# Performance work log

Hardware: AMD Instinct MI355X
Metric: run time of the kernel (lower is better)

## Reference

```python
import jax, jax.numpy as jnp
import numpy as np

N_NODES = 100000
N_EDGES = 1000000
D = 172          # n_node_features == memory_dimension (added together)
B = 4096         # batch after src/dst concat
K = 20           # n_neighbors


def setup_inputs() -> dict:
    key = jax.random.key(0)
    ks = jax.random.split(key, 12)
    return {
        "node_feats": jax.random.normal(ks[0], (N_NODES, D), dtype=jnp.float32),
        "edge_feats": jax.random.normal(ks[1], (N_EDGES, D), dtype=jnp.float32),
        "memory": jax.random.normal(ks[2], (N_NODES, D), dtype=jnp.float32),
        "timestamps": jax.random.uniform(ks[3], (B,), dtype=jnp.float32),
        "edge_times1": jax.random.uniform(ks[4], (B, K), dtype=jnp.float32),
        "edge_times2": jax.random.uniform(ks[5], (B * K, K), dtype=jnp.float32),
        "source_nodes": jax.random.randint(ks[6], (B,), 0, N_NODES),
        "neighbors1": jax.random.randint(ks[7], (B, K), 0, N_NODES),
        "edge_idxs1": jax.random.randint(ks[8], (B, K), 0, N_EDGES),
        "neighbors2": jax.random.randint(ks[9], (B * K, K), 0, N_NODES),
        "edge_idxs2": jax.random.randint(ks[10], (B * K, K), 0, N_EDGES),
    }


def reference(node_feats, edge_feats, memory, timestamps, edge_times1,
              edge_times2, source_nodes, neighbors1, edge_idxs1,
              neighbors2, edge_idxs2):
    # node_features[idx] + memory[idx] == (node_features + memory)[idx]
    node_mem = node_feats + memory  # [N, D]

    # ---- layer 0 data_collect ----
    src_feats1 = node_mem[source_nodes]        # [B, D]
    neigh_feats1 = node_mem[neighbors1]        # [B, K, D]
    edge_f1 = edge_feats[edge_idxs1]           # [B, K, D]
    deltas1 = timestamps[:, None] - edge_times1  # [B, K]
    mask1 = neighbors1 == 0                    # [B, K]

    # ---- layer 1 data_collect: nodes = neighbors.flatten(), ts repeated ----
    nodes2 = neighbors1.reshape(-1)            # [B*K]
    ts2 = jnp.repeat(timestamps, K)            # [B*K]
    src_feats2 = node_mem[nodes2]              # [B*K, D]
    neigh_feats2 = node_mem[neighbors2]        # [B*K, K, D]
    edge_f2 = edge_feats[edge_idxs2]           # [B*K, K, D]
    deltas2 = ts2[:, None] - edge_times2       # [B*K, K]
    mask2 = neighbors2 == 0                    # [B*K, K]

    return (src_feats1, neigh_feats1, edge_f1, deltas1, mask1,
            src_feats2, neigh_feats2, edge_f2, deltas2, mask2)
```

## Files before the change

### kernel.cpp

```cpp
#include <hip/hip_runtime.h>

typedef float f32x4 __attribute__((ext_vector_type(4)));

static constexpr unsigned D4 = 43;

__device__ __forceinline__ void nt_store4(f32x4* p, f32x4 v) {
    __builtin_nontemporal_store(v, p);
}

__global__ void addtab_k(f32x4* __restrict__ dst,
                         const f32x4* __restrict__ a,
                         const f32x4* __restrict__ b,
                         unsigned n4) {
    unsigned i = blockIdx.x * blockDim.x + threadIdx.x;
    unsigned stride = gridDim.x * blockDim.x;
    for (; i < n4; i += stride) {
        dst[i] = a[i] + b[i];
    }
}

__global__ void gather4_k(f32x4* __restrict__ dst,
                          const f32x4* __restrict__ a,
                          const int* __restrict__ idx,
                          unsigned n4) {
    unsigned i = blockIdx.x * blockDim.x + threadIdx.x;
    unsigned stride = gridDim.x * blockDim.x;
    for (; i < n4; i += stride) {
        unsigned row = i / D4;
        unsigned col = i - row * D4;
        unsigned s   = (unsigned)idx[row] * D4 + col;
        nt_store4(dst + i, a[s]);
    }
}

__global__ void gather4_dual_k(f32x4* __restrict__ dst1,
                               f32x4* __restrict__ dst2,
                               const f32x4* __restrict__ a,
                               const int* __restrict__ idx,
                               unsigned n4) {
    unsigned i = blockIdx.x * blockDim.x + threadIdx.x;
    unsigned stride = gridDim.x * blockDim.x;
    for (; i < n4; i += stride) {
        unsigned row = i / D4;
        unsigned col = i - row * D4;
        unsigned s   = (unsigned)idx[row] * D4 + col;
        f32x4 v = a[s];
        nt_store4(dst1 + i, v);
        nt_store4(dst2 + i, v);
    }
}

__global__ void gather_add4_k(f32x4* __restrict__ dst,
                              const f32x4* __restrict__ a,
                              const f32x4* __restrict__ b,
                              const int* __restrict__ idx,
                              unsigned n4) {
    unsigned i = blockIdx.x * blockDim.x + threadIdx.x;
    unsigned stride = gridDim.x * blockDim.x;
    for (; i < n4; i += stride) {
        unsigned row = i / D4;
        unsigned col = i - row * D4;
        unsigned s   = (unsigned)idx[row] * D4 + col;
        nt_store4(dst + i, a[s] + b[s]);
    }
}

__global__ void gather_add4_dual_k(f32x4* __restrict__ dst1,
                                   f32x4* __restrict__ dst2,
                                   const f32x4* __restrict__ a,
                                   const f32x4* __restrict__ b,
                                   const int* __restrict__ idx,
                                   unsigned n4) {
    unsigned i = blockIdx.x * blockDim.x + threadIdx.x;
    unsigned stride = gridDim.x * blockDim.x;
    for (; i < n4; i += stride) {
        unsigned row = i / D4;
        unsigned col = i - row * D4;
        unsigned s   = (unsigned)idx[row] * D4 + col;
        f32x4 v = a[s] + b[s];
        nt_store4(dst1 + i, v);
        nt_store4(dst2 + i, v);
    }
}

template <unsigned TSD>
__global__ void dm_k(float* __restrict__ deltas,
                     float* __restrict__ mask,
                     const float* __restrict__ ts,
                     const float* __restrict__ et,
                     const int* __restrict__ neigh,
                     unsigned n) {
    unsigned i = blockIdx.x * blockDim.x + threadIdx.x;
    unsigned stride = gridDim.x * blockDim.x;
    for (; i < n; i += stride) {
        __builtin_nontemporal_store(ts[i / TSD] - et[i], deltas + i);
        __builtin_nontemporal_store((neigh[i] == 0) ? 1.0f : 0.0f, mask + i);
    }
}

static inline unsigned grid_for(unsigned n, unsigned block, unsigned cap) {
    unsigned g = (n + block - 1) / block;
    return g < cap ? (g ? g : 1) : cap;
}

extern "C" void kernel_launch(void* const* d_in, const int* in_sizes, int n_in,
                              void* d_out, int out_size, void* d_ws, size_t ws_size,
                              hipStream_t stream) {
    const float* nf  = (const float*)d_in[0];
    const float* ef  = (const float*)d_in[1];
    const float* mem = (const float*)d_in[2];
    const float* ts  = (const float*)d_in[3];
    const float* et1 = (const float*)d_in[4];
    const float* et2 = (const float*)d_in[5];
    const int* srcn  = (const int*)d_in[6];
    const int* nb1   = (const int*)d_in[7];
    const int* ei1   = (const int*)d_in[8];
    const int* nb2   = (const int*)d_in[9];
    const int* ei2   = (const int*)d_in[10];

    constexpr unsigned B = 4096, K = 20, Dd = 172;
    constexpr unsigned BK = B * K;
    constexpr unsigned NN = 100000;

    float* out = (float*)d_out;
    size_t o = 0;
    float* src1 = out + o;  o += (size_t)B * Dd;
    float* nf1  = out + o;  o += (size_t)BK * Dd;
    float* ef1  = out + o;  o += (size_t)BK * Dd;
    float* dl1  = out + o;  o += (size_t)BK;
    float* mk1  = out + o;  o += (size_t)BK;
    float* sf2  = out + o;  o += (size_t)BK * Dd;
    float* nf2  = out + o;  o += (size_t)BK * K * Dd;
    float* ef2  = out + o;  o += (size_t)BK * K * Dd;
    float* dl2  = out + o;  o += (size_t)BK * K;
    float* mk2  = out + o;  o += (size_t)BK * K;

    const f32x4* nf4  = (const f32x4*)nf;
    const f32x4* mem4 = (const f32x4*)mem;
    const f32x4* ef4  = (const f32x4*)ef;

    const unsigned BLK = 256;
    const unsigned CAP = 2048;

    const size_t NM_BYTES = (size_t)NN * Dd * sizeof(float);

    if (ws_size >= NM_BYTES) {
        f32x4* nm4 = (f32x4*)d_ws;
        {
            unsigned n4 = NN * D4;
            addtab_k<<<grid_for(n4, BLK, CAP), BLK, 0, stream>>>(nm4, nf4, mem4, n4);
        }
        {
            unsigned n4 = B * D4;
            gather4_k<<<grid_for(n4, BLK, CAP), BLK, 0, stream>>>(
                (f32x4*)src1, nm4, srcn, n4);
        }
        {
            unsigned n4 = BK * D4;
            gather4_dual_k<<<grid_for(n4, BLK, CAP), BLK, 0, stream>>>(
                (f32x4*)nf1, (f32x4*)sf2, nm4, nb1, n4);
        }
        {
            unsigned n4 = BK * K * D4;
            gather4_k<<<grid_for(n4, BLK, CAP), BLK, 0, stream>>>(
                (f32x4*)nf2, nm4, nb2, n4);
        }
        dm_k<K><<<grid_for(BK, BLK, CAP), BLK, 0, stream>>>(dl1, mk1, ts, et1, nb1, BK);
        dm_k<K * K><<<grid_for(BK * K, BLK, CAP), BLK, 0, stream>>>(
            dl2, mk2, ts, et2, nb2, BK * K);
        {
            unsigned n4 = BK * D4;
            gather4_k<<<grid_for(n4, BLK, CAP), BLK, 0, stream>>>(
                (f32x4*)ef1, ef4, ei1, n4);
        }
        {
            unsigned n4 = BK * K * D4;
            gather4_k<<<grid_for(n4, BLK, CAP), BLK, 0, stream>>>(
                (f32x4*)ef2, ef4, ei2, n4);
        }
    } else {
        {
            unsigned n4 = B * D4;
            gather_add4_k<<<grid_for(n4, BLK, CAP), BLK, 0, stream>>>(
                (f32x4*)src1, nf4, mem4, srcn, n4);
        }
        {
            unsigned n4 = BK * D4;
            gather_add4_dual_k<<<grid_for(n4, BLK, CAP), BLK, 0, stream>>>(
                (f32x4*)nf1, (f32x4*)sf2, nf4, mem4, nb1, n4);
        }
        {
            unsigned n4 = BK * K * D4;
            gather_add4_k<<<grid_for(n4, BLK, CAP), BLK, 0, stream>>>(
                (f32x4*)nf2, nf4, mem4, nb2, n4);
        }
        dm_k<K><<<grid_for(BK, BLK, CAP), BLK, 0, stream>>>(dl1, mk1, ts, et1, nb1, BK);
        dm_k<K * K><<<grid_for(BK * K, BLK, CAP), BLK, 0, stream>>>(
            dl2, mk2, ts, et2, nb2, BK * K);
        {
            unsigned n4 = BK * D4;
            gather4_k<<<grid_for(n4, BLK, CAP), BLK, 0, stream>>>(
                (f32x4*)ef1, ef4, ei1, n4);
        }
        {
            unsigned n4 = BK * K * D4;
            gather4_k<<<grid_for(n4, BLK, CAP), BLK, 0, stream>>>(
                (f32x4*)ef2, ef4, ei2, n4);
        }
    }
}
```

Measured before the change: 804.8 us.

## Fuse independent stages into three block-partitioned kernels with exact grids

Replaces eight launches with three. The first kernel partitions its blocks across the node+memory table add, both delta/mask computations and the layer-1 edge gather. The second does all node-table gathers and the third does the large edge gather. Each uses one element per thread with exact grid sizes instead of capped grid-stride loops. This removes launch gaps and tail idle time and lets independent work overlap, but it relies on hardcoded problem sizes dividing evenly by 256 and removes the bounds checks.

```diff
diff --git a/kernel.cpp b/kernel.cpp
--- a/kernel.cpp
+++ b/kernel.cpp
@@ -4,20 +4,81 @@
 
 static constexpr unsigned D4 = 43;
 
-__device__ __forceinline__ void nt_store4(f32x4* p, f32x4 v) {
-    __builtin_nontemporal_store(v, p);
-}
-
-__global__ void addtab_k(f32x4* __restrict__ dst,
-                         const f32x4* __restrict__ a,
-                         const f32x4* __restrict__ b,
-                         unsigned n4) {
-    unsigned i = blockIdx.x * blockDim.x + threadIdx.x;
-    unsigned stride = gridDim.x * blockDim.x;
-    for (; i < n4; i += stride) {
-        dst[i] = a[i] + b[i];
-    }
-}
+
+__global__ __launch_bounds__(256) void k1_fused(
+    f32x4* __restrict__ nm, const f32x4* __restrict__ nf, const f32x4* __restrict__ mem,
+    float* __restrict__ dl1, float* __restrict__ mk1, const float* __restrict__ ts,
+    const float* __restrict__ et1, const int* __restrict__ nb1,
+    float* __restrict__ dl2, float* __restrict__ mk2,
+    const float* __restrict__ et2, const int* __restrict__ nb2,
+    f32x4* __restrict__ ef1o, const f32x4* __restrict__ ef, const int* __restrict__ ei1)
+{
+    constexpr unsigned ADD_N = 100000u * D4;
+    constexpr unsigned ADD_B = (ADD_N + 255u) / 256u;
+    constexpr unsigned DM1_B = 81920u / 256u;
+    constexpr unsigned DM2_B = 1638400u / 256u;
+    unsigned b = blockIdx.x, t = threadIdx.x;
+
+    if (b < ADD_B) {
+        unsigned i = b * 256u + t;
+        if (i < ADD_N) nm[i] = nf[i] + mem[i];
+    } else if (b < ADD_B + DM1_B) {
+        unsigned i = (b - ADD_B) * 256u + t;
+        __builtin_nontemporal_store(ts[i / 20u] - et1[i], dl1 + i);
+        __builtin_nontemporal_store((nb1[i] == 0) ? 1.0f : 0.0f, mk1 + i);
+    } else if (b < ADD_B + DM1_B + DM2_B) {
+        unsigned i = (b - ADD_B - DM1_B) * 256u + t;
+        __builtin_nontemporal_store(ts[i / 400u] - et2[i], dl2 + i);
+        __builtin_nontemporal_store((nb2[i] == 0) ? 1.0f : 0.0f, mk2 + i);
+    } else {
+        unsigned i = (b - ADD_B - DM1_B - DM2_B) * 256u + t;
+        unsigned row = i / D4, col = i - row * D4;
+        unsigned s = (unsigned)ei1[row] * D4 + col;
+        __builtin_nontemporal_store(ef[s], ef1o + i);
+    }
+}
+static constexpr unsigned K1_BLOCKS =
+    ((100000u * 43u + 255u) / 256u) + (81920u / 256u) + (1638400u / 256u)
+    + ((81920u * 43u) / 256u);
+
+__global__ __launch_bounds__(256) void k2_nodes(
+    const f32x4* __restrict__ nm,
+    f32x4* __restrict__ src1, const int* __restrict__ srcn,
+    f32x4* __restrict__ nf1o, f32x4* __restrict__ sf2, const int* __restrict__ nb1,
+    f32x4* __restrict__ nf2o, const int* __restrict__ nb2)
+{
+    constexpr unsigned S1_B = (4096u * D4) / 256u;
+    constexpr unsigned N1_B = (81920u * D4) / 256u;
+    unsigned b = blockIdx.x, t = threadIdx.x;
+
+    if (b < S1_B) {
+        unsigned i = b * 256u + t;
+        unsigned row = i / D4, col = i - row * D4;
+        __builtin_nontemporal_store(nm[(unsigned)srcn[row] * D4 + col], src1 + i);
+    } else if (b < S1_B + N1_B) {
+        unsigned i = (b - S1_B) * 256u + t;
+        unsigned row = i / D4, col = i - row * D4;
+        f32x4 v = nm[(unsigned)nb1[row] * D4 + col];
+        __builtin_nontemporal_store(v, nf1o + i);
+        __builtin_nontemporal_store(v, sf2 + i);
+    } else {
+        unsigned i = (b - S1_B - N1_B) * 256u + t;
+        unsigned row = i / D4, col = i - row * D4;
+        __builtin_nontemporal_store(nm[(unsigned)nb2[row] * D4 + col], nf2o + i);
+    }
+}
+static constexpr unsigned K2_BLOCKS =
+    ((4096u * 43u) / 256u) + ((81920u * 43u) / 256u) + ((1638400u * 43u) / 256u);
+
+__global__ __launch_bounds__(256) void k3_ef2(
+    f32x4* __restrict__ dst, const f32x4* __restrict__ ef, const int* __restrict__ ei2)
+{
+    unsigned i = blockIdx.x * 256u + threadIdx.x;
+    unsigned row = i / D4, col = i - row * D4;
+    __builtin_nontemporal_store(ef[(unsigned)ei2[row] * D4 + col], dst + i);
+}
+static constexpr unsigned K3_BLOCKS = (1638400u * 43u) / 256u;
+
 
 __global__ void gather4_k(f32x4* __restrict__ dst,
                           const f32x4* __restrict__ a,
@@ -26,27 +87,8 @@
     unsigned i = blockIdx.x * blockDim.x + threadIdx.x;
     unsigned stride = gridDim.x * blockDim.x;
     for (; i < n4; i += stride) {
-        unsigned row = i / D4;
-        unsigned col = i - row * D4;
-        unsigned s   = (unsigned)idx[row] * D4 + col;
-        nt_store4(dst + i, a[s]);
-    }
-}
-
-__global__ void gather4_dual_k(f32x4* __restrict__ dst1,
-                               f32x4* __restrict__ dst2,
-                               const f32x4* __restrict__ a,
-                               const int* __restrict__ idx,
-                               unsigned n4) {
-    unsigned i = blockIdx.x * blockDim.x + threadIdx.x;
-    unsigned stride = gridDim.x * blockDim.x;
-    for (; i < n4; i += stride) {
-        unsigned row = i / D4;
-        unsigned col = i - row * D4;
-        unsigned s   = (unsigned)idx[row] * D4 + col;
-        f32x4 v = a[s];
-        nt_store4(dst1 + i, v);
-        nt_store4(dst2 + i, v);
+        unsigned row = i / D4, col = i - row * D4;
+        __builtin_nontemporal_store(a[(unsigned)idx[row] * D4 + col], dst + i);
     }
 }
 
@@ -58,10 +100,9 @@
     unsigned i = blockIdx.x * blockDim.x + threadIdx.x;
     unsigned stride = gridDim.x * blockDim.x;
     for (; i < n4; i += stride) {
-        unsigned row = i / D4;
-        unsigned col = i - row * D4;
-        unsigned s   = (unsigned)idx[row] * D4 + col;
-        nt_store4(dst + i, a[s] + b[s]);
+        unsigned row = i / D4, col = i - row * D4;
+        unsigned s = (unsigned)idx[row] * D4 + col;
+        __builtin_nontemporal_store(a[s] + b[s], dst + i);
     }
 }
 
@@ -74,12 +115,11 @@
     unsigned i = blockIdx.x * blockDim.x + threadIdx.x;
     unsigned stride = gridDim.x * blockDim.x;
     for (; i < n4; i += stride) {
-        unsigned row = i / D4;
-        unsigned col = i - row * D4;
-        unsigned s   = (unsigned)idx[row] * D4 + col;
+        unsigned row = i / D4, col = i - row * D4;
+        unsigned s = (unsigned)idx[row] * D4 + col;
         f32x4 v = a[s] + b[s];
-        nt_store4(dst1 + i, v);
-        nt_store4(dst2 + i, v);
+        __builtin_nontemporal_store(v, dst1 + i);
+        __builtin_nontemporal_store(v, dst2 + i);
     }
 }
 
@@ -139,31 +179,37 @@
     const f32x4* mem4 = (const f32x4*)mem;
     const f32x4* ef4  = (const f32x4*)ef;
 
-    const unsigned BLK = 256;
-    const unsigned CAP = 2048;
-
     const size_t NM_BYTES = (size_t)NN * Dd * sizeof(float);
 
     if (ws_size >= NM_BYTES) {
         f32x4* nm4 = (f32x4*)d_ws;
-        {
-            unsigned n4 = NN * D4;
-            addtab_k<<<grid_for(n4, BLK, CAP), BLK, 0, stream>>>(nm4, nf4, mem4, n4);
-        }
+        k1_fused<<<K1_BLOCKS, 256, 0, stream>>>(
+            nm4, nf4, mem4,
+            dl1, mk1, ts, et1, nb1,
+            dl2, mk2, et2, nb2,
+            (f32x4*)ef1, ef4, ei1);
+        k2_nodes<<<K2_BLOCKS, 256, 0, stream>>>(
+            nm4,
+            (f32x4*)src1, srcn,
+            (f32x4*)nf1, (f32x4*)sf2, nb1,
+            (f32x4*)nf2, nb2);
+        k3_ef2<<<K3_BLOCKS, 256, 0, stream>>>((f32x4*)ef2, ef4, ei2);
+    } else {
+        const unsigned BLK = 256, CAP = 2048;
         {
             unsigned n4 = B * D4;
-            gather4_k<<<grid_for(n4, BLK, CAP), BLK, 0, stream>>>(
-                (f32x4*)src1, nm4, srcn, n4);
+            gather_add4_k<<<grid_for(n4, BLK, CAP), BLK, 0, stream>>>(
+                (f32x4*)src1, nf4, mem4, srcn, n4);
         }
         {
             unsigned n4 = BK * D4;
-            gather4_dual_k<<<grid_for(n4, BLK, CAP), BLK, 0, stream>>>(
-                (f32x4*)nf1, (f32x4*)sf2, nm4, nb1, n4);
+            gather_add4_dual_k<<<grid_for(n4, BLK, CAP), BLK, 0, stream>>>(
+                (f32x4*)nf1, (f32x4*)sf2, nf4, mem4, nb1, n4);
         }
         {
             unsigned n4 = BK * K * D4;
-            gather4_k<<<grid_for(n4, BLK, CAP), BLK, 0, stream>>>(
-                (f32x4*)nf2, nm4, nb2, n4);
+            gather_add4_k<<<grid_for(n4, BLK, CAP), BLK, 0, stream>>>(
+                (f32x4*)nf2, nf4, mem4, nb2, n4);
         }
         dm_k<K><<<grid_for(BK, BLK, CAP), BLK, 0, stream>>>(dl1, mk1, ts, et1, nb1, BK);
         dm_k<K * K><<<grid_for(BK * K, BLK, CAP), BLK, 0, stream>>>(
@@ -178,34 +224,5 @@
             gather4_k<<<grid_for(n4, BLK, CAP), BLK, 0, stream>>>(
                 (f32x4*)ef2, ef4, ei2, n4);
         }
-    } else {
-        {
-            unsigned n4 = B * D4;
-            gather_add4_k<<<grid_for(n4, BLK, CAP), BLK, 0, stream>>>(
-                (f32x4*)src1, nf4, mem4, srcn, n4);
-        }
-        {
-            unsigned n4 = BK * D4;
-            gather_add4_dual_k<<<grid_for(n4, BLK, CAP), BLK, 0, stream>>>(
-                (f32x4*)nf1, (f32x4*)sf2, nf4, mem4, nb1, n4);
-        }
-        {
-            unsigned n4 = BK * K * D4;
-            gather_add4_k<<<grid_for(n4, BLK, CAP), BLK, 0, stream>>>(
-                (f32x4*)nf2, nf4, mem4, nb2, n4);
-        }
-        dm_k<K><<<grid_for(BK, BLK, CAP), BLK, 0, stream>>>(dl1, mk1, ts, et1, nb1, BK);
-        dm_k<K * K><<<grid_for(BK * K, BLK, CAP), BLK, 0, stream>>>(
-            dl2, mk2, ts, et2, nb2, BK * K);
-        {
-            unsigned n4 = BK * D4;
-            gather4_k<<<grid_for(n4, BLK, CAP), BLK, 0, stream>>>(
-                (f32x4*)ef1, ef4, ei1, n4);
-        }
-        {
-            unsigned n4 = BK * K * D4;
-            gather4_k<<<grid_for(n4, BLK, CAP), BLK, 0, stream>>>(
-                (f32x4*)ef2, ef4, ei2, n4);
-        }
-    }
-}
+    }
+}
```

Result: no change. 802.5 us (-0.3%).
